# Optimization experiments

Measured on AMD Instinct MI355X. Metric: run time of the kernel, lower is better.

Reference implementation:

```python
import jax, jax.numpy as jnp
import numpy as np

NUM_CARDS = 40
NUM_SUITS = 4
SIDE_SUIT_LEN = 9
NUM_ACTIONS = 2 * NUM_CARDS + 1  # 81 (use_signals=True)
NUM_TRICKS = 10


def setup_inputs() -> dict:
    key = jax.random.key(0)
    ks = jax.random.split(key, 8)
    B, A, D_in, D_q = 16384, 40, 4096, 256
    backbone_embed = jax.random.normal(ks[0], (B, D_in), dtype=jnp.float32)
    rank = jax.random.randint(ks[1], (B, A), -1, SIDE_SUIT_LEN)
    # guarantee at least one valid action per row (slot 0)
    rank = rank.at[:, 0].set(jnp.maximum(rank[:, 0], 0))
    suit = jax.random.randint(ks[2], (B, A), 0, NUM_SUITS + 1)  # suit==NUM_SUITS -> no-signal action
    valid_actions = jnp.stack([rank, suit], axis=-1)
    phase = jax.random.randint(ks[3], (B,), 0, 2)
    trick = jax.random.randint(ks[4], (B,), 0, NUM_TRICKS)
    # params
    Wq = jax.random.normal(ks[5], (D_in, D_q), dtype=jnp.float32) / np.sqrt(D_in).astype(np.float32)
    bq = jnp.zeros((D_q,), jnp.float32)
    key_table = jax.random.normal(ks[6], (NUM_ACTIONS, D_q), dtype=jnp.float32)
    ln_gamma = jnp.ones((D_q,), jnp.float32)
    ln_beta = jnp.zeros((D_q,), jnp.float32)
    # signal_prior == 'lin': p_signal = 2 / (num_tricks_left + 1)
    num_left = NUM_TRICKS - jnp.arange(NUM_TRICKS, dtype=jnp.float32)
    p_signal = 2.0 / (num_left + 1.0)
    return dict(backbone_embed=backbone_embed, valid_actions=valid_actions, phase=phase,
                trick=trick, Wq=Wq, bq=bq, key_table=key_table, ln_gamma=ln_gamma,
                ln_beta=ln_beta, p_signal=p_signal)


def reference(backbone_embed, valid_actions, phase, trick, Wq, bq, key_table, ln_gamma, ln_beta, p_signal):
    D_q = Wq.shape[1]
    rank = valid_actions[..., 0]          # (B, A)
    suit = valid_actions[..., 1]          # (B, A)
    aidx = phase[:, None] * NUM_CARDS + suit * SIDE_SUIT_LEN + rank
    aidx = jnp.where(rank == -1, -1, jnp.where(suit == NUM_SUITS, 2 * NUM_CARDS, aidx))
    # PaddedEmbed: shift by 1, row 0 is the zero padding row for idx == -1
    table = jnp.concatenate([jnp.zeros((1, D_q), key_table.dtype), key_table], axis=0)
    k = table[aidx + 1]                   # (B, A, D_q)
    # LayerNorm over last dim
    mu = k.mean(axis=-1, keepdims=True)
    var = k.var(axis=-1, keepdims=True)
    k = (k - mu) * jax.lax.rsqrt(var + 1e-5) * ln_gamma + ln_beta
    q = backbone_embed @ Wq + bq          # (B, D_q)
    attn = jnp.einsum('bq,baq->ba', q, k) / jnp.sqrt(jnp.float32(D_q))
    attn = jnp.where(rank == -1, -jnp.inf, attn)
    # no-signal bias on action 0 during signal phase
    n_valid = (rank != -1).sum(axis=-1).astype(jnp.float32)
    ps = p_signal[trick]
    w = jnp.log(jnp.maximum((1.0 - ps) / ps * (n_valid - 1.0), 1e-5))
    w = jnp.where(n_valid == 1.0, 0.0, w)
    attn = attn.at[:, 0].add(jnp.where(phase == 1, w, 0.0))
    return jax.nn.log_softmax(attn, axis=-1)
```

## Files before the change

kernel.cpp:

```cpp
#include <hip/hip_runtime.h>
#include <hip/hip_bf16.h>
#include <math.h>


typedef _Float16 half8_t __attribute__((ext_vector_type(8)));
typedef float    f32x4_t __attribute__((ext_vector_type(4)));

#define NUM_B 16384
#define D_IN  4096
#define D_Q   256
#define N_ACT 40
#define NPAD  96

__device__ __forceinline__ half8_t cvt8(const float4 a, const float4 b) {
  half8_t h;
  h[0] = (_Float16)a.x; h[1] = (_Float16)a.y; h[2] = (_Float16)a.z; h[3] = (_Float16)a.w;
  h[4] = (_Float16)b.x; h[5] = (_Float16)b.y; h[6] = (_Float16)b.z; h[7] = (_Float16)b.w;
  return h;
}
__device__ __forceinline__ void gl_lds16f(const float* g, float* l) {
  __builtin_amdgcn_global_load_lds(
      (const __attribute__((address_space(1))) void*)g,
      (__attribute__((address_space(3))) void*)l, 16, 0, 0);
}
__device__ __forceinline__ void gl_lds16h(const _Float16* g, _Float16* l) {
  __builtin_amdgcn_global_load_lds(
      (const __attribute__((address_space(1))) void*)g,
      (__attribute__((address_space(3))) void*)l, 16, 0, 0);
}

__global__ __launch_bounds__(256) void ln_table_k(const float* __restrict__ kt,
                                                  const float* __restrict__ gamma,
                                                  const float* __restrict__ beta,
                                                  const float* __restrict__ bq,
                                                  float* __restrict__ out,
                                                  float* __restrict__ bqk) {
  __shared__ float red[8];
  __shared__ float red2[4];
  const int t = threadIdx.x, r = blockIdx.x;
  float v = kt[r * 256 + t];
  float s = v, sq = v * v;
#pragma unroll
  for (int off = 1; off < 64; off <<= 1) {
    s  += __shfl_xor(s, off);
    sq += __shfl_xor(sq, off);
  }
  if ((t & 63) == 0) { red[t >> 6] = s; red[4 + (t >> 6)] = sq; }
  __syncthreads();
  s  = red[0] + red[1] + red[2] + red[3];
  sq = red[4] + red[5] + red[6] + red[7];
  const float mu  = s * (1.0f / 256.0f);
  const float var = sq * (1.0f / 256.0f) - mu * mu;
  const float inv = 1.0f / sqrtf(var + 1e-5f);
  const float o = (v - mu) * inv * gamma[t] + beta[t];
  out[r * 256 + t] = o;
  float p = o * bq[t];
#pragma unroll
  for (int off = 1; off < 64; off <<= 1) p += __shfl_xor(p, off);
  if ((t & 63) == 0) red2[t >> 6] = p;
  __syncthreads();
  if (t == 0) bqk[r] = red2[0] + red2[1] + red2[2] + red2[3];
}

__global__ __launch_bounds__(256) void wk_gemm_k(const float* __restrict__ Wq,
                                                 const float* __restrict__ tbl,
                                                 _Float16* __restrict__ Bf) {
  const int lane = threadIdx.x & 63, w = threadIdx.x >> 6;
  const int wm = w >> 1, wn = w & 1;
  const int m0 = blockIdx.x * 64 + wm * 32;
  const int n0 = wn * 48;
  const int fr = lane & 15, fg = lane >> 4;
  f32x4_t acc[2][3] = {};
  for (int k0 = 0; k0 < 256; k0 += 32) {
    half8_t af[2], bf[3];
#pragma unroll
    for (int i = 0; i < 2; ++i) {
      const float* p = Wq + (size_t)(m0 + i * 16 + fr) * D_Q + k0 + fg * 8;
      af[i] = cvt8(*(const float4*)p, *(const float4*)(p + 4));
    }
#pragma unroll
    for (int j = 0; j < 3; ++j) {
      const int n = n0 + j * 16 + fr;
      if (n < 81) {
        const float* p = tbl + (size_t)n * D_Q + k0 + fg * 8;
        bf[j] = cvt8(*(const float4*)p, *(const float4*)(p + 4));
      } else {
        bf[j] = (half8_t)(_Float16)0.0f;
      }
    }
#pragma unroll
    for (int i = 0; i < 2; ++i)
#pragma unroll
      for (int j = 0; j < 3; ++j)
        acc[i][j] = __builtin_amdgcn_mfma_f32_16x16x32_f16(af[i], bf[j], acc[i][j], 0, 0, 0);
  }
#pragma unroll
  for (int i = 0; i < 2; ++i)
#pragma unroll
    for (int j = 0; j < 3; ++j)
#pragma unroll
      for (int r = 0; r < 4; ++r) {
        const int k = m0 + i * 16 + fg * 4 + r;
        const int n = n0 + j * 16 + fr;
        Bf[(((size_t)(k >> 5) * 6 + (n >> 4)) * 64 +
            (((k >> 3) & 3) * 16 + (n & 15))) * 8 + (k & 7)] =
            (_Float16)acc[i][j][r];
      }
}

__global__ __launch_bounds__(512) void gemm_part_k(const float* __restrict__ A,
                                                   const _Float16* __restrict__ Bf,
                                                   float* __restrict__ part) {
  __shared__ __align__(16) char smem[45056];
  float*    Afs = (float*)smem;
  _Float16* Bls = (_Float16*)(smem + 32768);

  const int t = threadIdx.x, lane = t & 63, w = t >> 6;
  const int fr = lane & 15, fg = lane >> 4;
  const int ks = blockIdx.y;
  const size_t row0 = (size_t)blockIdx.x * 128;
  const int k0 = ks * 1024;

#define STAGE(T, P)                                                           \
  do {                                                                        \
    _Pragma("unroll") for (int q_ = 0; q_ < 3; ++q_) {                        \
      const int id_ = w * 3 + q_;                                             \
      if (id_ < 16) {                                                         \
        const int r_ = id_ * 8 + (lane >> 3);                                 \
        gl_lds16f(A + (size_t)(row0 + r_) * D_IN + k0 + (T)*32 +              \
                      (((lane & 7) ^ (r_ & 7)) << 2),                         \
                  Afs + (P)*4096 + id_ * 256);                                \
      } else if (id_ < 22) {                                                  \
        const int jg_ = id_ - 16;                                             \
        gl_lds16h(Bf + ((size_t)(ks * 32 + (T)) * 6 + jg_) * 512 + lane * 8,  \
                  Bls + (P)*3072 + jg_ * 512);                                \
      }                                                                       \
    }                                                                         \
  } while (0)

  const int wm = w >> 1, wn = w & 1;
  int aoff[2][2];
#pragma unroll
  for (int i = 0; i < 2; ++i)
#pragma unroll
    for (int h = 0; h < 2; ++h) {
      const int R = wm * 32 + i * 16 + fr;
      aoff[i][h] = R * 32 + (((fg * 2 + h) ^ (R & 7)) << 2);
    }
  int boff[3];
#pragma unroll
  for (int j = 0; j < 3; ++j) boff[j] = (wn * 3 + j) * 512 + lane * 8;

  f32x4_t acc[2][3] = {};

  STAGE(0, 0);
  for (int kt = 0; kt < 32; ++kt) {
    if (kt < 31) STAGE(kt + 1, (kt + 1) & 1);
    __builtin_amdgcn_sched_barrier(0);
    if (kt < 31) {
      if (w < 7) asm volatile("s_waitcnt vmcnt(3)" ::: "memory");
      else       asm volatile("s_waitcnt vmcnt(1)" ::: "memory");
    } else {
      asm volatile("s_waitcnt vmcnt(0)" ::: "memory");
    }
    __builtin_amdgcn_s_barrier();
    __builtin_amdgcn_sched_barrier(0);

    const float*    Ap = Afs + (kt & 1) * 4096;
    const _Float16* Bp = Bls + (kt & 1) * 3072;
    half8_t bfv[3];
#pragma unroll
    for (int j = 0; j < 3; ++j) bfv[j] = *(const half8_t*)(Bp + boff[j]);
#pragma unroll
    for (int i = 0; i < 2; ++i) {
      const float4 x0 = *(const float4*)(Ap + aoff[i][0]);
      const float4 x1 = *(const float4*)(Ap + aoff[i][1]);
      const half8_t af = cvt8(x0, x1);
#pragma unroll
      for (int j = 0; j < 3; ++j)
        acc[i][j] = __builtin_amdgcn_mfma_f32_16x16x32_f16(af, bfv[j], acc[i][j], 0, 0, 0);
    }
    asm volatile("s_waitcnt lgkmcnt(0)" ::: "memory");
    __builtin_amdgcn_s_barrier();
    __builtin_amdgcn_sched_barrier(0);
  }
#undef STAGE

  float* pb = part + ((size_t)ks * NUM_B + row0) * NPAD;
#pragma unroll
  for (int i = 0; i < 2; ++i)
#pragma unroll
    for (int j = 0; j < 3; ++j) {
      const int col = wn * 48 + j * 16 + fr;
#pragma unroll
      for (int r = 0; r < 4; ++r)
        pb[(size_t)(wm * 32 + i * 16 + fg * 4 + r) * NPAD + col] = acc[i][j][r];
    }
}

__global__ __launch_bounds__(256) void softmax_k(const float* __restrict__ part,
                                                 const float* __restrict__ bqk,
                                                 const int* __restrict__ va,
                                                 const int* __restrict__ phase,
                                                 const int* __restrict__ trick,
                                                 const float* __restrict__ psig,
                                                 float* __restrict__ out) {
  const int t = threadIdx.x;
  const int lane = t & 63, w = t >> 6;
  const int b = blockIdx.x * 4 + w;

  float sx = 0.f, sy = 0.f;
  if (lane < 48) {
#pragma unroll
    for (int ks = 0; ks < 4; ++ks) {
      const float2 v = *(const float2*)&part[((size_t)ks * NUM_B + b) * NPAD + lane * 2];
      sx += v.x; sy += v.y;
    }
  }

  int rank = -1, suit = 0;
  if (lane < N_ACT) {
    rank = va[((size_t)b * N_ACT + lane) * 2];
    suit = va[((size_t)b * N_ACT + lane) * 2 + 1];
  }
  const int ph = phase[b];
  const bool valid = (rank >= 0);
  const int aidx = valid ? (suit == 4 ? 80 : ph * 40 + suit * 9 + rank) : -1;
  const int nvalid = __popcll(__ballot(valid));

  const int srcl = valid ? (aidx >> 1) : 0;
  const float v0 = __shfl(sx, srcl);
  const float v1 = __shfl(sy, srcl);

  float attn_l = -INFINITY;
  if (valid) attn_l = (((aidx & 1) ? v1 : v0) + bqk[aidx]) * 0.0625f;

  if (ph == 1 && lane == 0) {
    const float ps = psig[trick[b]];
    const float nv = (float)nvalid;
    const float wv = (nv == 1.0f) ? 0.0f
                                  : logf(fmaxf((1.0f - ps) / ps * (nv - 1.0f), 1e-5f));
    attn_l += wv;
  }

  float m = attn_l;
#pragma unroll
  for (int off = 1; off < 64; off <<= 1) m = fmaxf(m, __shfl_xor(m, off));
  const float e = expf(attn_l - m);
  float ssum = e;
#pragma unroll
  for (int off = 1; off < 64; off <<= 1) ssum += __shfl_xor(ssum, off);
  const float o = attn_l - m - logf(ssum);
  if (lane < N_ACT) out[(size_t)b * N_ACT + lane] = valid ? o : -3.0e38f;
}

extern "C" void kernel_launch(void* const* d_in, const int* in_sizes, int n_in,
                              void* d_out, int out_size, void* d_ws, size_t ws_size,
                              hipStream_t stream) {
  const float* backbone = (const float*)d_in[0];
  const int*   va       = (const int*)d_in[1];
  const int*   phase    = (const int*)d_in[2];
  const int*   trick    = (const int*)d_in[3];
  const float* Wq       = (const float*)d_in[4];
  const float* bq       = (const float*)d_in[5];
  const float* keytab   = (const float*)d_in[6];
  const float* gamma    = (const float*)d_in[7];
  const float* beta     = (const float*)d_in[8];
  const float* psig     = (const float*)d_in[9];
  float* out = (float*)d_out;

  char* ws = (char*)d_ws;
  _Float16* Bf   = (_Float16*)ws;
  float* tableLN = (float*)(ws + (1u << 20));
  float* bqk     = (float*)(ws + (1u << 20) + (128u << 10));
  float* part    = (float*)(ws + (2u << 20));

  ln_table_k<<<dim3(81), 256, 0, stream>>>(keytab, gamma, beta, bq, tableLN, bqk);
  wk_gemm_k<<<dim3(64), 256, 0, stream>>>(Wq, tableLN, Bf);
  gemm_part_k<<<dim3(NUM_B / 128, 4), 512, 0, stream>>>(backbone, Bf, part);
  softmax_k<<<dim3(NUM_B / 4), 256, 0, stream>>>(part, bqk, va, phase, trick,
                                                 psig, out);
}
```

Measured before the change: 92.00 us.

## Stage A tiles in 64-wide K super-steps spread across two iterations

The split-K GEMM kernel now loads the fp32 activation tile as 64-column super-tiles, double-buffered in a larger LDS region. Each half of a super-tile is issued in one of two consecutive iterations, while B keeps its per-iteration double buffer. This spreads the A loads evenly over all 8 waves and lets them be issued further ahead of use, with the wait counts adjusted to match. The trade is roughly 76KB of LDS per block instead of 44KB, which may limit how many blocks fit per CU.

```diff
diff --git a/kernel.cpp b/kernel.cpp
--- a/kernel.cpp
+++ b/kernel.cpp
@@ -111,9 +111,9 @@
 __global__ __launch_bounds__(512) void gemm_part_k(const float* __restrict__ A,
                                                    const _Float16* __restrict__ Bf,
                                                    float* __restrict__ part) {
-  __shared__ __align__(16) char smem[45056];
+  __shared__ __align__(16) char smem[77824];
   float*    Afs = (float*)smem;
-  _Float16* Bls = (_Float16*)(smem + 32768);
+  _Float16* Bls = (_Float16*)(smem + 65536);
 
   const int t = threadIdx.x, lane = t & 63, w = t >> 6;
   const int fr = lane & 15, fg = lane >> 4;
@@ -121,60 +121,75 @@
   const size_t row0 = (size_t)blockIdx.x * 128;
   const int k0 = ks * 1024;
 
-#define STAGE(T, P)                                                           \
+#define STAGE_B(TB)                                                           \
   do {                                                                        \
-    _Pragma("unroll") for (int q_ = 0; q_ < 3; ++q_) {                        \
-      const int id_ = w * 3 + q_;                                             \
-      if (id_ < 16) {                                                         \
-        const int r_ = id_ * 8 + (lane >> 3);                                 \
-        gl_lds16f(A + (size_t)(row0 + r_) * D_IN + k0 + (T)*32 +              \
-                      (((lane & 7) ^ (r_ & 7)) << 2),                         \
-                  Afs + (P)*4096 + id_ * 256);                                \
-      } else if (id_ < 22) {                                                  \
-        const int jg_ = id_ - 16;                                             \
-        gl_lds16h(Bf + ((size_t)(ks * 32 + (T)) * 6 + jg_) * 512 + lane * 8,  \
-                  Bls + (P)*3072 + jg_ * 512);                                \
-      }                                                                       \
+    if (w < 6)                                                                \
+      gl_lds16h(Bf + ((size_t)(ks * 32 + (TB)) * 6 + w) * 512 + lane * 8,     \
+                Bls + ((TB)&1) * 3072 + w * 512);                             \
+  } while (0)
+#define STAGE_A(SU, HF)                                                       \
+  do {                                                                        \
+    float* abase = Afs + ((SU)&1) * 8192;                                     \
+    _Pragma("unroll") for (int q_ = 0; q_ < 2; ++q_) {                        \
+      const int gid_ = (HF)*16 + w * 2 + q_;                                  \
+      const int r_ = gid_ * 4 + (lane >> 4);                                  \
+      gl_lds16f(A + (size_t)(row0 + r_) * D_IN + k0 + (SU)*64 +               \
+                    (((lane & 15) ^ (r_ & 7)) << 2),                          \
+                abase + gid_ * 256);                                          \
     }                                                                         \
   } while (0)
 
   const int wm = w >> 1, wn = w & 1;
-  int aoff[2][2];
+  int aoff[2][2][2];
 #pragma unroll
   for (int i = 0; i < 2; ++i)
 #pragma unroll
-    for (int h = 0; h < 2; ++h) {
-      const int R = wm * 32 + i * 16 + fr;
-      aoff[i][h] = R * 32 + (((fg * 2 + h) ^ (R & 7)) << 2);
-    }
+    for (int kh = 0; kh < 2; ++kh)
+#pragma unroll
+      for (int h = 0; h < 2; ++h) {
+        const int R = wm * 32 + i * 16 + fr;
+        aoff[i][kh][h] = R * 64 + (((kh * 8 + fg * 2 + h) ^ (R & 7)) << 2);
+      }
   int boff[3];
 #pragma unroll
   for (int j = 0; j < 3; ++j) boff[j] = (wn * 3 + j) * 512 + lane * 8;
 
   f32x4_t acc[2][3] = {};
 
-  STAGE(0, 0);
+  STAGE_B(0);
+  STAGE_A(0, 0);
+  STAGE_A(0, 1);
+  __builtin_amdgcn_sched_barrier(0);
+  asm volatile("s_waitcnt vmcnt(0)" ::: "memory");
+  __builtin_amdgcn_s_barrier();
+  __builtin_amdgcn_sched_barrier(0);
+
   for (int kt = 0; kt < 32; ++kt) {
-    if (kt < 31) STAGE(kt + 1, (kt + 1) & 1);
+    if (kt < 31) STAGE_B(kt + 1);
+    if (kt < 30) STAGE_A((kt >> 1) + 1, kt & 1);
     __builtin_amdgcn_sched_barrier(0);
-    if (kt < 31) {
-      if (w < 7) asm volatile("s_waitcnt vmcnt(3)" ::: "memory");
-      else       asm volatile("s_waitcnt vmcnt(1)" ::: "memory");
+    if (kt < 30) {
+      if (w < 6) asm volatile("s_waitcnt vmcnt(3)" ::: "memory");
+      else       asm volatile("s_waitcnt vmcnt(2)" ::: "memory");
+    } else if (kt == 30) {
+      if (w < 6) asm volatile("s_waitcnt vmcnt(1)" ::: "memory");
+      else       asm volatile("s_waitcnt vmcnt(0)" ::: "memory");
     } else {
       asm volatile("s_waitcnt vmcnt(0)" ::: "memory");
     }
     __builtin_amdgcn_s_barrier();
     __builtin_amdgcn_sched_barrier(0);
 
-    const float*    Ap = Afs + (kt & 1) * 4096;
+    const float*    Ap = Afs + ((kt >> 1) & 1) * 8192;
     const _Float16* Bp = Bls + (kt & 1) * 3072;
+    const int kh = kt & 1;
     half8_t bfv[3];
 #pragma unroll
     for (int j = 0; j < 3; ++j) bfv[j] = *(const half8_t*)(Bp + boff[j]);
 #pragma unroll
     for (int i = 0; i < 2; ++i) {
-      const float4 x0 = *(const float4*)(Ap + aoff[i][0]);
-      const float4 x1 = *(const float4*)(Ap + aoff[i][1]);
+      const float4 x0 = *(const float4*)(Ap + aoff[i][kh][0]);
+      const float4 x1 = *(const float4*)(Ap + aoff[i][kh][1]);
       const half8_t af = cvt8(x0, x1);
 #pragma unroll
       for (int j = 0; j < 3; ++j)
@@ -184,7 +199,8 @@
     __builtin_amdgcn_s_barrier();
     __builtin_amdgcn_sched_barrier(0);
   }
-#undef STAGE
+#undef STAGE_A
+#undef STAGE_B
 
   float* pb = part + ((size_t)ks * NUM_B + row0) * NPAD;
 #pragma unroll
```

After: 92.80 us. No clear change (+0.9%).
